# Kernel optimization log

Measured on AMD Instinct MI355X. Metric: run time of the kernel, lower is better.

## Reference

```python
import jax, jax.numpy as jnp
import numpy as np

N = 50000       # nodes
E = 800000      # edges (avg degree 16)
IN_DIM = 64
H = 64          # hidden_dim
OUT_DIM = 64
R = 8           # n_relations
L = 3           # n_layers
LN_EPS = 1e-5
NEG_SLOPE = 0.2


def _layer_norm(x, g, b):
    mu = jnp.mean(x, axis=-1, keepdims=True)
    var = jnp.mean((x - mu) ** 2, axis=-1, keepdims=True)
    return (x - mu) * jax.lax.rsqrt(var + LN_EPS) * g + b


def setup_inputs() -> dict:
    key = jax.random.key(0)
    ks = jax.random.split(key, 10)
    s = 0.05
    return {
        "x": jax.random.normal(ks[0], (N, IN_DIM), jnp.float32),
        "edge_index": jax.random.randint(ks[1], (2, E), 0, N),
        "edge_type": jax.random.randint(ks[2], (E,), 0, R),
        "W_in": jax.random.normal(ks[3], (H, IN_DIM), jnp.float32) * s,
        "b_in": jnp.zeros((H,), jnp.float32),
        "W_rel": jax.random.normal(ks[4], (R, H, H), jnp.float32) * s,   # no bias
        "W_gate": jax.random.normal(ks[5], (R, H, H), jnp.float32) * s,
        "b_gate": jnp.zeros((R, H), jnp.float32),
        "W_att": jax.random.normal(ks[6], (R, 2 * H), jnp.float32) * s,  # Linear(2H,1) per relation
        "b_att": jnp.zeros((R,), jnp.float32),
        "ln_gamma": jnp.ones((L, H), jnp.float32),
        "ln_beta": jnp.zeros((L, H), jnp.float32),
        "W_out": jax.random.normal(ks[7], (OUT_DIM, H), jnp.float32) * s,
        "b_out": jnp.zeros((OUT_DIM,), jnp.float32),
    }


def reference(x, edge_index, edge_type, W_in, b_in, W_rel, W_gate, b_gate,
              W_att, b_att, ln_gamma, ln_beta, W_out, b_out):
    src, dst = edge_index[0], edge_index[1]
    Wa_src, Wa_dst = W_att[:, :H], W_att[:, H:]      # [R,H] each
    seg = dst * R + edge_type                        # combined (node, relation) scatter key
    eidx = jnp.arange(E)

    h = jax.nn.relu(x @ W_in.T + b_in)               # [N,H]

    for layer in range(L):
        h_src = h[src]                               # [E,H] gather
        h_dst = h[dst]                               # [E,H] gather
        # attention score of each edge under its own relation's Linear(2H,1)
        scores_all = h_src @ Wa_src.T + h_dst @ Wa_dst.T + b_att   # [E,R]
        scores = scores_all[eidx, edge_type]                        # [E]
        scores = jax.nn.leaky_relu(scores, NEG_SLOPE)
        # softmax over dim=0 within each relation's edge set (as in the torch code)
        m = jax.ops.segment_max(scores, edge_type, num_segments=R)
        ex = jnp.exp(scores - m[edge_type])
        denom = jax.ops.segment_sum(ex, edge_type, num_segments=R)
        att = ex / denom[edge_type]                                 # [E]
        # relation-specific linear of source features (linear commutes with gather)
        hWr = jnp.einsum('nh,rkh->nrk', h, W_rel)                   # [N,R,H]
        msg = hWr[src, edge_type] * att[:, None]                    # [E,H]
        # per-relation scatter-add into destinations
        agg = jax.ops.segment_sum(msg, seg, num_segments=N * R)     # [N*R,H]
        agg = agg.reshape(N, R, H)
        gate = jax.nn.sigmoid(jnp.einsum('nh,rkh->nrk', h, W_gate) + b_gate)  # [N,R,H]
        h_new = jnp.mean(gate * agg, axis=1)         # sum(messages)/n_relations
        h = jax.nn.relu(_layer_norm(h + h_new, ln_gamma[layer], ln_beta[layer]))

    return h @ W_out.T + b_out
```

## Files before the change

kernel.cpp:

```cpp
#include <hip/hip_runtime.h>
#include <math.h>

#define NN 50000
#define EE 800000
#define HH 64
#define RR 8
#define LL 3
#define NR (NN * RR)
#define NB ((NR + 255) / 256)
#define LN_EPS 1e-5f
#define NEG_SLOPE 0.2f
#define LDH 68
#define PNB 584
#define OTB (16 * LDH)
#define DSPREAD 64

typedef __attribute__((ext_vector_type(8))) short bf8;
typedef __attribute__((ext_vector_type(4))) float f4;
typedef __attribute__((ext_vector_type(8))) unsigned short us8;
typedef __attribute__((ext_vector_type(2))) unsigned int u2;

__device__ __forceinline__ unsigned short bf16r(float f) {
    unsigned u = __float_as_uint(f);
    unsigned r = u + 0x7fffu + ((u >> 16) & 1u);
    return (unsigned short)(r >> 16);
}
__device__ __forceinline__ float bf2f(unsigned short u) {
    return __uint_as_float(((unsigned)u) << 16);
}

__global__ __launch_bounds__(256) void proj_in(
    const float* __restrict__ x, const float* __restrict__ W,
    const float* __restrict__ bias, const unsigned short* __restrict__ WaB,
    float* __restrict__ h, unsigned short* __restrict__ hbf,
    float* __restrict__ s_src, float* __restrict__ s_dst) {
    __shared__ float WT[64 * LDH];
    __shared__ float xs[16 * LDH];
    __shared__ float hs[16 * LDH];
    int tid = threadIdx.x;
    int n0 = blockIdx.x * 16;
    #pragma unroll
    for (int s = 0; s < 16; ++s) {
        int idx = tid + 256 * s;
        int k = idx >> 6, i = idx & 63;
        WT[i * LDH + k] = W[idx];
    }
    int row = tid >> 4, cg = tid & 15;
    {
        f4 v = ((const f4*)x)[(size_t)(n0 + row) * 16 + cg];
        *(f4*)&xs[row * LDH + cg * 4] = v;
    }
    __syncthreads();
    f4 acc;
    {
        f4 b = *(const f4*)(bias + cg * 4);
        acc = b;
        #pragma unroll
        for (int i = 0; i < 64; ++i) {
            float xv = xs[row * LDH + i];
            f4 wt = *(const f4*)&WT[i * LDH + cg * 4];
            acc[0] += xv * wt[0];
            acc[1] += xv * wt[1];
            acc[2] += xv * wt[2];
            acc[3] += xv * wt[3];
        }
        #pragma unroll
        for (int j = 0; j < 4; ++j) acc[j] = fmaxf(acc[j], 0.f);
        int n = n0 + row;
        *(f4*)(h + (size_t)n * 64 + cg * 4) = acc;
        u2 u;
        u[0] = (unsigned)bf16r(acc[0]) | ((unsigned)bf16r(acc[1]) << 16);
        u[1] = (unsigned)bf16r(acc[2]) | ((unsigned)bf16r(acc[3]) << 16);
        *(u2*)(hbf + (size_t)n * 64 + cg * 4) = u;
        *(f4*)&hs[row * LDH + cg * 4] = acc;
    }
    __syncthreads();
    if (tid < 64) {
        int lane = tid;
        int quad = lane >> 4, lr = lane & 15;
        f4 sc = (f4){0.f, 0.f, 0.f, 0.f};
        #pragma unroll
        for (int kb = 0; kb < 2; ++kb) {
            const float* p = &hs[lr * LDH + kb * 32 + quad * 8];
            bf8 a;
            #pragma unroll
            for (int j = 0; j < 8; ++j) a[j] = (short)bf16r(p[j]);
            const bf8* bw = (const bf8*)(WaB + lr * 64 + kb * 32 + quad * 8);
            sc = __builtin_amdgcn_mfma_f32_16x16x32_bf16(a, *bw, sc, 0, 0, 0);
        }
        #pragma unroll
        for (int j = 0; j < 4; ++j) {
            int n = n0 + quad * 4 + j;
            if (lr < 8) s_src[n * 8 + lr] = sc[j];
            else        s_dst[n * 8 + (lr - 8)] = sc[j];
        }
    }
}

__global__ void edge_count(const int* __restrict__ ei, const int* __restrict__ et,
                           int* __restrict__ counts, int* __restrict__ rank) {
    int e = blockIdx.x * 256 + threadIdx.x;
    int d = ei[EE + e], t = et[e];
    rank[e] = atomicAdd(&counts[d * 8 + t], 1);
}

__global__ void scan1(const int* __restrict__ counts, int* __restrict__ offs,
                      int* __restrict__ bsum) {
    __shared__ int s[256];
    int tid = threadIdx.x;
    int i = blockIdx.x * 256 + tid;
    int v = (i < NR) ? counts[i] : 0;
    s[tid] = v; __syncthreads();
    for (int d = 1; d < 256; d <<= 1) {
        int x = (tid >= d) ? s[tid - d] : 0;
        __syncthreads();
        s[tid] += x;
        __syncthreads();
    }
    if (i < NR) offs[i] = s[tid] - v;
    if (tid == 255) bsum[blockIdx.x] = s[255];
}

__global__ void scan2(int* __restrict__ bsum) {
    __shared__ int s[1024];
    int tid = threadIdx.x;
    int carry = 0;
    for (int c0 = 0; c0 < NB; c0 += 1024) {
        int i = c0 + tid;
        int v = (i < NB) ? bsum[i] : 0;
        s[tid] = v; __syncthreads();
        for (int d = 1; d < 1024; d <<= 1) {
            int x = (tid >= d) ? s[tid - d] : 0;
            __syncthreads();
            s[tid] += x;
            __syncthreads();
        }
        if (i < NB) bsum[i] = carry + s[tid] - v;
        int tot = s[1023];
        __syncthreads();
        carry += tot;
    }
}

__global__ void edge_fill(const int* __restrict__ ei, const int* __restrict__ et,
                          const int* __restrict__ rank, const int* __restrict__ offs,
                          const int* __restrict__ bsum, u2* __restrict__ spack) {
    int e = blockIdx.x * 256 + threadIdx.x;
    int s = ei[e], d = ei[EE + e], t = et[e];
    int seg = d * 8 + t;
    int slot = offs[seg] + bsum[seg >> 8] + rank[e];
    spack[slot] = (u2){(unsigned)s, (unsigned)seg};
}

__global__ void cvt_w(const float* __restrict__ Wr, const float* __restrict__ Wg,
                      const float* __restrict__ Wa, const float* __restrict__ Wo,
                      unsigned short* __restrict__ WrB, unsigned short* __restrict__ WgB,
                      unsigned short* __restrict__ WaB, unsigned short* __restrict__ WoB) {
    int i = blockIdx.x * 256 + threadIdx.x;
    WrB[i] = bf16r(Wr[i]);
    WgB[i] = bf16r(Wg[i]);
    if (i < 1024) {
        int row = i >> 6, k = i & 63;
        float v = (row < 8) ? Wa[row * 128 + k] : Wa[(row - 8) * 128 + 64 + k];
        WaB[i] = bf16r(v);
    }
    if (i < 4096) WoB[i] = bf16r(Wo[i]);
}

__global__ void edge_softmax2(const u2* __restrict__ spack,
                              const float* __restrict__ s_src, const float* __restrict__ s_dst,
                              const float* __restrict__ b_att,
                              u2* __restrict__ epack, float* __restrict__ dpart) {
    __shared__ float lsum[4][8];
    int tid = threadIdx.x;
    if (tid < 32) lsum[tid >> 3][tid & 7] = 0.f;
    __syncthreads();
    int slot = blockIdx.x * 256 + tid;
    u2 sp = spack[slot];
    int src = (int)sp[0];
    int seg = (int)sp[1];
    int t = seg & 7;
    float sc = s_src[src * 8 + t] + s_dst[seg] + b_att[t];
    sc = (sc >= 0.f) ? sc : NEG_SLOPE * sc;
    float ex = __expf(sc);
    epack[slot] = (u2){(unsigned)src, __float_as_uint(ex)};
    atomicAdd(&lsum[tid >> 6][t], ex);
    __syncthreads();
    if (tid < 8) {
        float v = lsum[0][tid] + lsum[1][tid] + lsum[2][tid] + lsum[3][tid];
        atomicAdd(&dpart[(blockIdx.x & (DSPREAD - 1)) * 16 + tid], v);
    }
}

template<bool EMIT, bool OUT>
__global__ __launch_bounds__(256, 6) void combine_fused(
    const float* __restrict__ hbuf, const unsigned short* __restrict__ hbf_in,
    const int* __restrict__ offs, const int* __restrict__ bsum,
    const u2* __restrict__ epack, const float* __restrict__ dpartL,
    const unsigned short* __restrict__ WrB, const unsigned short* __restrict__ WgB,
    const unsigned short* __restrict__ WaB, const unsigned short* __restrict__ WoB,
    const float* __restrict__ b_gate, const float* __restrict__ gamma,
    const float* __restrict__ beta, float* __restrict__ hout,
    unsigned short* __restrict__ hbf_out, float* __restrict__ ssrc_out,
    float* __restrict__ sdst_out, float* __restrict__ outp,
    const float* __restrict__ b_out) {
    __shared__ float hs[16 * LDH];
    __shared__ alignas(16) unsigned short ps[16 * PNB];
    __shared__ float idn8[8];
    __shared__ int offsL[129];
    float* ps_f = (float*)ps;
    int tid = threadIdx.x;
    int n0 = blockIdx.x * 16;

    {
        int row = tid >> 4, c4 = tid & 15;
        f4 v = ((const f4*)hbuf)[(size_t)(n0 + row) * 16 + c4];
        *(f4*)&hs[row * LDH + c4 * 4] = v;
    }
    if (tid < 129) {
        int sidx = n0 * 8 + tid;
        offsL[tid] = (sidx < NR) ? (offs[sidx] + bsum[sidx >> 8]) : EE;
    }
    if (tid >= 192) {
        int t = tid & 7, g = (tid - 192) >> 3;
        float sm = 0.f;
        #pragma unroll
        for (int j = 0; j < 8; ++j) sm += dpartL[(g * 8 + j) * 16 + t];
        sm += __shfl_xor(sm, 8, 64);
        sm += __shfl_xor(sm, 16, 64);
        sm += __shfl_xor(sm, 32, 64);
        if ((tid & 63) < 8) idn8[t] = 1.f / sm;
    }
    __syncthreads();

    {
        int segl = tid >> 1;
        int half = tid & 1;
        int lo = offsL[segl], hi = offsL[segl + 1];
        int r = segl & 7;
        int gn = segl >> 3;
        float fa[32];
        #pragma unroll
        for (int j = 0; j < 32; ++j) fa[j] = 0.f;
        for (int s = lo; s < hi; s += 2) {
            u2 pk0 = epack[s];
            int s1 = (s + 1 < hi) ? (s + 1) : s;
            u2 pk1 = epack[s1];
            float a0 = __uint_as_float(pk0[1]);
            float a1 = (s + 1 < hi) ? __uint_as_float(pk1[1]) : 0.f;
            const us8* hp0 = (const us8*)(hbf_in + ((size_t)(int)pk0[0] << 6) + half * 32);
            const us8* hp1 = (const us8*)(hbf_in + ((size_t)(int)pk1[0] << 6) + half * 32);
            #pragma unroll
            for (int q = 0; q < 4; ++q) {
                us8 v0 = hp0[q];
                us8 v1 = hp1[q];
                #pragma unroll
                for (int j = 0; j < 8; ++j) {
                    fa[q * 8 + j] += a0 * bf2f(v0[j]);
                    fa[q * 8 + j] += a1 * bf2f(v1[j]);
                }
            }
        }
        float sA = idn8[r];
        unsigned short* pp = &ps[gn * PNB + r * 72 + half * 32];
        #pragma unroll
        for (int q = 0; q < 4; ++q) {
            us8 o;
            #pragma unroll
            for (int j = 0; j < 8; ++j) o[j] = bf16r(fa[q * 8 + j] * sA);
            *(us8*)(pp + q * 8) = o;
        }
    }
    __syncthreads();

    int w = tid >> 6, lane = tid & 63;
    int quad = lane >> 4, lr = lane & 15;
    int tn = w;

    bf8 a_h[2];
    #pragma unroll
    for (int kb = 0; kb < 2; ++kb) {
        const float* p = &hs[lr * LDH + kb * 32 + quad * 8];
        bf8 a;
        #pragma unroll
        for (int j = 0; j < 8; ++j) a[j] = (short)bf16r(p[j]);
        a_h[kb] = a;
    }

    f4 acc = (f4){0.f, 0.f, 0.f, 0.f};
    for (int r = 0; r < 8; ++r) {
        bf8 a_p[2];
        #pragma unroll
        for (int kb = 0; kb < 2; ++kb)
            a_p[kb] = *(const bf8*)&ps[lr * PNB + r * 72 + kb * 32 + quad * 8];
        f4 aggc = (f4){0.f, 0.f, 0.f, 0.f};
        f4 gacc = (f4){0.f, 0.f, 0.f, 0.f};
        #pragma unroll
        for (int kb = 0; kb < 2; ++kb) {
            const bf8* br = (const bf8*)(WrB + ((r * 64 + tn * 16 + lr) * 64 + kb * 32 + quad * 8));
            const bf8* bg = (const bf8*)(WgB + ((r * 64 + tn * 16 + lr) * 64 + kb * 32 + quad * 8));
            aggc = __builtin_amdgcn_mfma_f32_16x16x32_bf16(a_p[kb], *br, aggc, 0, 0, 0);
            gacc = __builtin_amdgcn_mfma_f32_16x16x32_bf16(a_h[kb], *bg, gacc, 0, 0, 0);
        }
        float bg = b_gate[r * 64 + tn * 16 + lr];
        #pragma unroll
        for (int j = 0; j < 4; ++j) {
            float g = 1.f / (1.f + __expf(-(gacc[j] + bg)));
            acc[j] += g * aggc[j];
        }
    }
    __syncthreads();

    #pragma unroll
    for (int j = 0; j < 4; ++j) {
        int row = quad * 4 + j;
        int col = tn * 16 + lr;
        ps_f[row * LDH + col] = hs[row * LDH + col] + acc[j] * 0.125f;
    }
    __syncthreads();

    {
        int row = tid >> 4, c = tid & 15;
        int n = n0 + row;
        f4 tv = *(const f4*)&ps_f[row * LDH + c * 4];
        float s1 = tv[0] + tv[1] + tv[2] + tv[3];
        float s2 = tv[0]*tv[0] + tv[1]*tv[1] + tv[2]*tv[2] + tv[3]*tv[3];
        #pragma unroll
        for (int off = 1; off <= 8; off <<= 1) {
            s1 += __shfl_xor(s1, off, 64);
            s2 += __shfl_xor(s2, off, 64);
        }
        float mu = s1 * (1.f / 64.f);
        float var = s2 * (1.f / 64.f) - mu * mu;
        float rs = rsqrtf(var + LN_EPS);
        f4 g = *(const f4*)(gamma + c * 4);
        f4 b = *(const f4*)(beta + c * 4);
        f4 ov;
        #pragma unroll
        for (int j = 0; j < 4; ++j)
            ov[j] = fmaxf((tv[j] - mu) * rs * g[j] + b[j], 0.f);
        if (!OUT)
            *(f4*)(hout + (size_t)n * 64 + c * 4) = ov;
        *(f4*)&ps_f[OTB + row * LDH + c * 4] = ov;
        if (EMIT) {
            u2 u;
            u[0] = (unsigned)bf16r(ov[0]) | ((unsigned)bf16r(ov[1]) << 16);
            u[1] = (unsigned)bf16r(ov[2]) | ((unsigned)bf16r(ov[3]) << 16);
            *(u2*)(hbf_out + (size_t)n * 64 + c * 4) = u;
        }
    }

    if (EMIT) {
        __syncthreads();
        if (w == 0) {
            f4 sc = (f4){0.f, 0.f, 0.f, 0.f};
            #pragma unroll
            for (int kb = 0; kb < 2; ++kb) {
                const float* p = &ps_f[OTB + lr * LDH + kb * 32 + quad * 8];
                bf8 a;
                #pragma unroll
                for (int j = 0; j < 8; ++j) a[j] = (short)bf16r(p[j]);
                const bf8* bw = (const bf8*)(WaB + lr * 64 + kb * 32 + quad * 8);
                sc = __builtin_amdgcn_mfma_f32_16x16x32_bf16(a, *bw, sc, 0, 0, 0);
            }
            #pragma unroll
            for (int j = 0; j < 4; ++j) {
                int n = n0 + quad * 4 + j;
                if (lr < 8) ssrc_out[n * 8 + lr] = sc[j];
                else        sdst_out[n * 8 + (lr - 8)] = sc[j];
            }
        }
    }

    if (OUT) {
        __syncthreads();
        f4 oc = (f4){0.f, 0.f, 0.f, 0.f};
        #pragma unroll
        for (int kb = 0; kb < 2; ++kb) {
            const float* p = &ps_f[OTB + lr * LDH + kb * 32 + quad * 8];
            bf8 a;
            #pragma unroll
            for (int j = 0; j < 8; ++j) a[j] = (short)bf16r(p[j]);
            const bf8* bw = (const bf8*)(WoB + ((tn * 16 + lr) * 64 + kb * 32 + quad * 8));
            oc = __builtin_amdgcn_mfma_f32_16x16x32_bf16(a, *bw, oc, 0, 0, 0);
        }
        float bo = b_out[tn * 16 + lr];
        #pragma unroll
        for (int j = 0; j < 4; ++j)
            outp[(size_t)(n0 + quad * 4 + j) * 64 + tn * 16 + lr] = oc[j] + bo;
    }
}

extern "C" void kernel_launch(void* const* d_in, const int* in_sizes, int n_in,
                              void* d_out, int out_size, void* d_ws, size_t ws_size,
                              hipStream_t stream) {
    const float* x      = (const float*)d_in[0];
    const int*   ei     = (const int*)d_in[1];
    const int*   et     = (const int*)d_in[2];
    const float* W_in   = (const float*)d_in[3];
    const float* b_in   = (const float*)d_in[4];
    const float* W_rel  = (const float*)d_in[5];
    const float* W_gate = (const float*)d_in[6];
    const float* b_gate = (const float*)d_in[7];
    const float* W_att  = (const float*)d_in[8];
    const float* b_att  = (const float*)d_in[9];
    const float* ln_g   = (const float*)d_in[10];
    const float* ln_b   = (const float*)d_in[11];
    const float* W_out  = (const float*)d_in[12];
    const float* b_out  = (const float*)d_in[13];
    float* out = (float*)d_out;

    float* h0 = (float*)d_out;

    char* ws = (char*)d_ws;
    float* h1 = (float*)ws;                     ws += (size_t)NN * 64 * 4;
    unsigned short* hbfA = (unsigned short*)ws; ws += (size_t)NN * 64 * 2;
    unsigned short* hbfB = (unsigned short*)ws; ws += (size_t)NN * 64 * 2;
    float* s_src = (float*)ws;                  ws += (size_t)NN * 8 * 4;
    float* s_dst = (float*)ws;                  ws += (size_t)NN * 8 * 4;
    unsigned short* WrB = (unsigned short*)ws;  ws += (size_t)RR * 64 * 64 * 2;
    unsigned short* WgB = (unsigned short*)ws;  ws += (size_t)RR * 64 * 64 * 2;
    unsigned short* WaB = (unsigned short*)ws;  ws += 2048;
    unsigned short* WoB = (unsigned short*)ws;  ws += 8192;
    int* counts = (int*)ws;                     ws += (size_t)NR * 4;
    float* dpart = (float*)ws;                  ws += 3 * DSPREAD * 16 * 4;
    int* offs = (int*)ws;                       ws += (size_t)NR * 4;
    int* bsum = (int*)ws;                       ws += 6400;
    int* rank = (int*)ws;                       ws += (size_t)EE * 4;
    u2* spack = (u2*)ws;                        ws += (size_t)EE * 8;
    u2* epack = (u2*)ws;                        ws += (size_t)EE * 8;

    hipMemsetAsync(counts, 0, (size_t)NR * 4 + 3 * DSPREAD * 16 * 4, stream);
    cvt_w<<<128, 256, 0, stream>>>(W_rel, W_gate, W_att, W_out, WrB, WgB, WaB, WoB);
    edge_count<<<EE / 256, 256, 0, stream>>>(ei, et, counts, rank);
    scan1<<<NB, 256, 0, stream>>>(counts, offs, bsum);
    scan2<<<1, 1024, 0, stream>>>(bsum);
    edge_fill<<<EE / 256, 256, 0, stream>>>(ei, et, rank, offs, bsum, spack);
    proj_in<<<NN / 16, 256, 0, stream>>>(x, W_in, b_in, WaB, h0, hbfA, s_src, s_dst);

    const int tiles16 = NN / 16;
    float* hA = h0;  float* hB = h1;
    unsigned short* bfA = hbfA;  unsigned short* bfB = hbfB;
    for (int layer = 0; layer < LL; ++layer) {
        float* dpl = dpart + (size_t)layer * DSPREAD * 16;
        edge_softmax2<<<EE / 256, 256, 0, stream>>>(spack, s_src, s_dst, b_att,
                                                    epack, dpl);
        if (layer < LL - 1) {
            combine_fused<true, false><<<tiles16, 256, 0, stream>>>(
                hA, bfA, offs, bsum, epack, dpl, WrB, WgB, WaB, WoB, b_gate,
                ln_g + layer * 64, ln_b + layer * 64,
                hB, bfB, s_src, s_dst, out, b_out);
        } else {
            combine_fused<false, true><<<tiles16, 256, 0, stream>>>(
                hA, bfA, offs, bsum, epack, dpl, WrB, WgB, WaB, WoB, b_gate,
                ln_g + layer * 64, ln_b + layer * 64,
                hB, bfB, s_src, s_dst, out, b_out);
        }
        float* tf = hA; hA = hB; hB = tf;
        unsigned short* tb = bfA; bfA = bfB; bfB = tb;
    }
}
```

Baseline: 420.2 us.

## Aggregate edge messages per block with shared-memory atomics instead of per-segment threads

The combine kernel now assigns one thread per edge across the block's whole edge range and accumulates weighted source features into a shared fp32 tile [128 segments x 66] with LDS atomics. This replaces the old scheme where each pair of threads walked one (node, relation) segment serially. The goal is to fix load imbalance from uneven segment lengths. The softmax kernel now writes only the exp values, and the source index is read from the existing spack. In exchange there are 64 LDS atomic adds per edge, a larger shared buffer, and occupancy is lowered to 4 waves via launch bounds.

```diff
diff --git a/kernel.cpp b/kernel.cpp
--- a/kernel.cpp
+++ b/kernel.cpp
@@ -14,9 +14,11 @@
 #define PNB 584
 #define OTB (16 * LDH)
 #define DSPREAD 64
+#define SAG 66
 
 typedef __attribute__((ext_vector_type(8))) short bf8;
 typedef __attribute__((ext_vector_type(4))) float f4;
+typedef __attribute__((ext_vector_type(2))) float f2;
 typedef __attribute__((ext_vector_type(8))) unsigned short us8;
 typedef __attribute__((ext_vector_type(2))) unsigned int u2;
 
@@ -170,7 +172,7 @@
 __global__ void edge_softmax2(const u2* __restrict__ spack,
                               const float* __restrict__ s_src, const float* __restrict__ s_dst,
                               const float* __restrict__ b_att,
-                              u2* __restrict__ epack, float* __restrict__ dpart) {
+                              float* __restrict__ exw, float* __restrict__ dpart) {
     __shared__ float lsum[4][8];
     int tid = threadIdx.x;
     if (tid < 32) lsum[tid >> 3][tid & 7] = 0.f;
@@ -183,7 +185,7 @@
     float sc = s_src[src * 8 + t] + s_dst[seg] + b_att[t];
     sc = (sc >= 0.f) ? sc : NEG_SLOPE * sc;
     float ex = __expf(sc);
-    epack[slot] = (u2){(unsigned)src, __float_as_uint(ex)};
+    exw[slot] = ex;
     atomicAdd(&lsum[tid >> 6][t], ex);
     __syncthreads();
     if (tid < 8) {
@@ -193,10 +195,11 @@
 }
 
 template<bool EMIT, bool OUT>
-__global__ __launch_bounds__(256, 6) void combine_fused(
+__global__ __launch_bounds__(256, 4) void combine_fused(
     const float* __restrict__ hbuf, const unsigned short* __restrict__ hbf_in,
     const int* __restrict__ offs, const int* __restrict__ bsum,
-    const u2* __restrict__ epack, const float* __restrict__ dpartL,
+    const u2* __restrict__ spack, const float* __restrict__ exw,
+    const float* __restrict__ dpartL,
     const unsigned short* __restrict__ WrB, const unsigned short* __restrict__ WgB,
     const unsigned short* __restrict__ WaB, const unsigned short* __restrict__ WoB,
     const float* __restrict__ b_gate, const float* __restrict__ gamma,
@@ -205,10 +208,11 @@
     float* __restrict__ sdst_out, float* __restrict__ outp,
     const float* __restrict__ b_out) {
     __shared__ float hs[16 * LDH];
-    __shared__ alignas(16) unsigned short ps[16 * PNB];
+    __shared__ alignas(16) float agg[128 * SAG];
     __shared__ float idn8[8];
-    __shared__ int offsL[129];
-    float* ps_f = (float*)ps;
+    __shared__ int rng[2];
+    unsigned short* ps = (unsigned short*)agg;
+    float* ps_f = agg;
     int tid = threadIdx.x;
     int n0 = blockIdx.x * 16;
 
@@ -217,9 +221,9 @@
         f4 v = ((const f4*)hbuf)[(size_t)(n0 + row) * 16 + c4];
         *(f4*)&hs[row * LDH + c4 * 4] = v;
     }
-    if (tid < 129) {
-        int sidx = n0 * 8 + tid;
-        offsL[tid] = (sidx < NR) ? (offs[sidx] + bsum[sidx >> 8]) : EE;
+    if (tid < 2) {
+        int sidx = n0 * 8 + tid * 128;
+        rng[tid] = (sidx < NR) ? (offs[sidx] + bsum[sidx >> 8]) : EE;
     }
     if (tid >= 192) {
         int t = tid & 7, g = (tid - 192) >> 3;
@@ -231,43 +235,53 @@
         sm += __shfl_xor(sm, 32, 64);
         if ((tid & 63) < 8) idn8[t] = 1.f / sm;
     }
-    __syncthreads();
-
-    {
-        int segl = tid >> 1;
-        int half = tid & 1;
-        int lo = offsL[segl], hi = offsL[segl + 1];
-        int r = segl & 7;
-        int gn = segl >> 3;
-        float fa[32];
-        #pragma unroll
-        for (int j = 0; j < 32; ++j) fa[j] = 0.f;
-        for (int s = lo; s < hi; s += 2) {
-            u2 pk0 = epack[s];
-            int s1 = (s + 1 < hi) ? (s + 1) : s;
-            u2 pk1 = epack[s1];
-            float a0 = __uint_as_float(pk0[1]);
-            float a1 = (s + 1 < hi) ? __uint_as_float(pk1[1]) : 0.f;
-            const us8* hp0 = (const us8*)(hbf_in + ((size_t)(int)pk0[0] << 6) + half * 32);
-            const us8* hp1 = (const us8*)(hbf_in + ((size_t)(int)pk1[0] << 6) + half * 32);
-            #pragma unroll
-            for (int q = 0; q < 4; ++q) {
-                us8 v0 = hp0[q];
-                us8 v1 = hp1[q];
+    {
+        f4 z = (f4){0.f, 0.f, 0.f, 0.f};
+        for (int i = tid; i < (128 * SAG) / 4; i += 256) ((f4*)agg)[i] = z;
+    }
+    __syncthreads();
+
+    {
+        int lo0 = rng[0], hi0 = rng[1];
+        for (int s = lo0 + tid; s < hi0; s += 256) {
+            u2 sp = spack[s];
+            int src = (int)sp[0];
+            int abase = ((int)sp[1] - n0 * 8) * SAG;
+            float ex = exw[s];
+            const us8* hp = (const us8*)(hbf_in + ((size_t)src << 6));
+            #pragma unroll
+            for (int q = 0; q < 8; ++q) {
+                us8 v = hp[q];
                 #pragma unroll
-                for (int j = 0; j < 8; ++j) {
-                    fa[q * 8 + j] += a0 * bf2f(v0[j]);
-                    fa[q * 8 + j] += a1 * bf2f(v1[j]);
-                }
+                for (int j = 0; j < 8; ++j)
+                    atomicAdd(&agg[abase + q * 8 + j], ex * bf2f(v[j]));
             }
         }
+    }
+    __syncthreads();
+
+    float fr[32];
+    {
+        int segl = tid >> 1, half = tid & 1;
+        const float* ar = &agg[segl * SAG + half * 32];
+        #pragma unroll
+        for (int j = 0; j < 16; ++j) {
+            f2 v = *(const f2*)(ar + 2 * j);
+            fr[2 * j]     = v[0];
+            fr[2 * j + 1] = v[1];
+        }
+    }
+    __syncthreads();
+    {
+        int segl = tid >> 1, half = tid & 1;
+        int r = segl & 7, gn = segl >> 3;
         float sA = idn8[r];
         unsigned short* pp = &ps[gn * PNB + r * 72 + half * 32];
         #pragma unroll
         for (int q = 0; q < 4; ++q) {
             us8 o;
             #pragma unroll
-            for (int j = 0; j < 8; ++j) o[j] = bf16r(fa[q * 8 + j] * sA);
+            for (int j = 0; j < 8; ++j) o[j] = bf16r(fr[q * 8 + j] * sA);
             *(us8*)(pp + q * 8) = o;
         }
     }
@@ -428,7 +442,7 @@
     int* bsum = (int*)ws;                       ws += 6400;
     int* rank = (int*)ws;                       ws += (size_t)EE * 4;
     u2* spack = (u2*)ws;                        ws += (size_t)EE * 8;
-    u2* epack = (u2*)ws;                        ws += (size_t)EE * 8;
+    float* exw = (float*)ws;                    ws += (size_t)EE * 4;
 
     hipMemsetAsync(counts, 0, (size_t)NR * 4 + 3 * DSPREAD * 16 * 4, stream);
     cvt_w<<<128, 256, 0, stream>>>(W_rel, W_gate, W_att, W_out, WrB, WgB, WaB, WoB);
@@ -444,15 +458,15 @@
     for (int layer = 0; layer < LL; ++layer) {
         float* dpl = dpart + (size_t)layer * DSPREAD * 16;
         edge_softmax2<<<EE / 256, 256, 0, stream>>>(spack, s_src, s_dst, b_att,
-                                                    epack, dpl);
+                                                    exw, dpl);
         if (layer < LL - 1) {
             combine_fused<true, false><<<tiles16, 256, 0, stream>>>(
-                hA, bfA, offs, bsum, epack, dpl, WrB, WgB, WaB, WoB, b_gate,
+                hA, bfA, offs, bsum, spack, exw, dpl, WrB, WgB, WaB, WoB, b_gate,
                 ln_g + layer * 64, ln_b + layer * 64,
                 hB, bfB, s_src, s_dst, out, b_out);
         } else {
             combine_fused<false, true><<<tiles16, 256, 0, stream>>>(
-                hA, bfA, offs, bsum, epack, dpl, WrB, WgB, WaB, WoB, b_gate,
+                hA, bfA, offs, bsum, spack, exw, dpl, WrB, WgB, WaB, WoB, b_gate,
                 ln_g + layer * 64, ln_b + layer * 64,
                 hB, bfB, s_src, s_dst, out, b_out);
         }
```

Result: slower. 1.228 ms (+192.2%).

## Split fused combine into separate gather kernel and dense MFMA combine kernel

Applied to the files above, without the earlier changes.

The edge gather/aggregation phase moves out of the fused combine kernel into a new gather_seg kernel. It writes per-(node,relation) aggregated bf16 rows to a global buffer, which combine_dense then reads directly as MFMA operands. The gather also unpacks bf16 pairs with bit masks into float2 FMAs. The split frees LDS and registers in each kernel, which may raise occupancy and separate irregular memory traffic from dense compute. In exchange it adds a global round trip of N*R*64 bf16 values and an extra launch per layer.

```diff
diff --git a/kernel.cpp b/kernel.cpp
--- a/kernel.cpp
+++ b/kernel.cpp
@@ -11,14 +11,15 @@
 #define LN_EPS 1e-5f
 #define NEG_SLOPE 0.2f
 #define LDH 68
-#define PNB 584
 #define OTB (16 * LDH)
 #define DSPREAD 64
 
 typedef __attribute__((ext_vector_type(8))) short bf8;
 typedef __attribute__((ext_vector_type(4))) float f4;
+typedef __attribute__((ext_vector_type(2))) float f2;
 typedef __attribute__((ext_vector_type(8))) unsigned short us8;
 typedef __attribute__((ext_vector_type(2))) unsigned int u2;
+typedef __attribute__((ext_vector_type(4))) unsigned int u4;
 
 __device__ __forceinline__ unsigned short bf16r(float f) {
     unsigned u = __float_as_uint(f);
@@ -192,11 +193,77 @@
     }
 }
 
-template<bool EMIT, bool OUT>
-__global__ __launch_bounds__(256, 6) void combine_fused(
-    const float* __restrict__ hbuf, const unsigned short* __restrict__ hbf_in,
+__global__ __launch_bounds__(256, 6) void gather_seg(
     const int* __restrict__ offs, const int* __restrict__ bsum,
     const u2* __restrict__ epack, const float* __restrict__ dpartL,
+    const unsigned short* __restrict__ hbf_in,
+    unsigned short* __restrict__ psG) {
+    int tid = threadIdx.x;
+    int segl = tid >> 1, half = tid & 1;
+    int sidx = blockIdx.x * 128 + segl;
+    int lo = offs[sidx] + bsum[sidx >> 8];
+    int nxt = sidx + 1;
+    int hi = (nxt < NR) ? (offs[nxt] + bsum[nxt >> 8]) : EE;
+
+    int lane = tid & 63;
+    float sm = 0.f;
+    #pragma unroll
+    for (int k = 0; k < 8; ++k)
+        sm += dpartL[(((lane >> 3) + 8 * k) * 16) + (lane & 7)];
+    sm += __shfl_xor(sm, 8, 64);
+    sm += __shfl_xor(sm, 16, 64);
+    sm += __shfl_xor(sm, 32, 64);
+    float rc = 1.f / sm;
+    float idn = __shfl(rc, segl & 7, 64);
+
+    f2 acc[16];
+    #pragma unroll
+    for (int i = 0; i < 16; ++i) acc[i] = (f2){0.f, 0.f};
+
+    for (int s = lo; s < hi; s += 2) {
+        u2 pk0 = epack[s];
+        int s1 = (s + 1 < hi) ? (s + 1) : s;
+        u2 pk1 = epack[s1];
+        float a0 = __uint_as_float(pk0[1]);
+        float a1 = (s + 1 < hi) ? __uint_as_float(pk1[1]) : 0.f;
+        const u4* hp0 = (const u4*)(hbf_in + ((size_t)(int)pk0[0] << 6) + half * 32);
+        const u4* hp1 = (const u4*)(hbf_in + ((size_t)(int)pk1[0] << 6) + half * 32);
+        f2 va0 = (f2){a0, a0};
+        f2 va1 = (f2){a1, a1};
+        #pragma unroll
+        for (int q = 0; q < 4; ++q) {
+            u4 d0 = hp0[q];
+            u4 d1 = hp1[q];
+            #pragma unroll
+            for (int k = 0; k < 4; ++k) {
+                f2 w0, w1;
+                w0[0] = __uint_as_float(d0[k] << 16);
+                w0[1] = __uint_as_float(d0[k] & 0xffff0000u);
+                w1[0] = __uint_as_float(d1[k] << 16);
+                w1[1] = __uint_as_float(d1[k] & 0xffff0000u);
+                acc[q * 4 + k] += va0 * w0;
+                acc[q * 4 + k] += va1 * w1;
+            }
+        }
+    }
+
+    int gn = segl >> 3, r = segl & 7;
+    unsigned short* pp = psG + ((((size_t)blockIdx.x * 16 + gn) * 8 + r) << 6) + half * 32;
+    #pragma unroll
+    for (int q = 0; q < 4; ++q) {
+        us8 o;
+        #pragma unroll
+        for (int k = 0; k < 4; ++k) {
+            o[2 * k]     = bf16r(acc[q * 4 + k][0] * idn);
+            o[2 * k + 1] = bf16r(acc[q * 4 + k][1] * idn);
+        }
+        *(us8*)(pp + q * 8) = o;
+    }
+}
+
+template<bool EMIT, bool OUT>
+__global__ __launch_bounds__(256, 6) void combine_dense(
+    const float* __restrict__ hbuf, const unsigned short* __restrict__ psG,
     const unsigned short* __restrict__ WrB, const unsigned short* __restrict__ WgB,
     const unsigned short* __restrict__ WaB, const unsigned short* __restrict__ WoB,
     const float* __restrict__ b_gate, const float* __restrict__ gamma,
@@ -205,10 +272,7 @@
     float* __restrict__ sdst_out, float* __restrict__ outp,
     const float* __restrict__ b_out) {
     __shared__ float hs[16 * LDH];
-    __shared__ alignas(16) unsigned short ps[16 * PNB];
-    __shared__ float idn8[8];
-    __shared__ int offsL[129];
-    float* ps_f = (float*)ps;
+    __shared__ float tf[32 * LDH];
     int tid = threadIdx.x;
     int n0 = blockIdx.x * 16;
 
@@ -217,60 +281,6 @@
         f4 v = ((const f4*)hbuf)[(size_t)(n0 + row) * 16 + c4];
         *(f4*)&hs[row * LDH + c4 * 4] = v;
     }
-    if (tid < 129) {
-        int sidx = n0 * 8 + tid;
-        offsL[tid] = (sidx < NR) ? (offs[sidx] + bsum[sidx >> 8]) : EE;
-    }
-    if (tid >= 192) {
-        int t = tid & 7, g = (tid - 192) >> 3;
-        float sm = 0.f;
-        #pragma unroll
-        for (int j = 0; j < 8; ++j) sm += dpartL[(g * 8 + j) * 16 + t];
-        sm += __shfl_xor(sm, 8, 64);
-        sm += __shfl_xor(sm, 16, 64);
-        sm += __shfl_xor(sm, 32, 64);
-        if ((tid & 63) < 8) idn8[t] = 1.f / sm;
-    }
-    __syncthreads();
-
-    {
-        int segl = tid >> 1;
-        int half = tid & 1;
-        int lo = offsL[segl], hi = offsL[segl + 1];
-        int r = segl & 7;
-        int gn = segl >> 3;
-        float fa[32];
-        #pragma unroll
-        for (int j = 0; j < 32; ++j) fa[j] = 0.f;
-        for (int s = lo; s < hi; s += 2) {
-            u2 pk0 = epack[s];
-            int s1 = (s + 1 < hi) ? (s + 1) : s;
-            u2 pk1 = epack[s1];
-            float a0 = __uint_as_float(pk0[1]);
-            float a1 = (s + 1 < hi) ? __uint_as_float(pk1[1]) : 0.f;
-            const us8* hp0 = (const us8*)(hbf_in + ((size_t)(int)pk0[0] << 6) + half * 32);
-            const us8* hp1 = (const us8*)(hbf_in + ((size_t)(int)pk1[0] << 6) + half * 32);
-            #pragma unroll
-            for (int q = 0; q < 4; ++q) {
-                us8 v0 = hp0[q];
-                us8 v1 = hp1[q];
-                #pragma unroll
-                for (int j = 0; j < 8; ++j) {
-                    fa[q * 8 + j] += a0 * bf2f(v0[j]);
-                    fa[q * 8 + j] += a1 * bf2f(v1[j]);
-                }
-            }
-        }
-        float sA = idn8[r];
-        unsigned short* pp = &ps[gn * PNB + r * 72 + half * 32];
-        #pragma unroll
-        for (int q = 0; q < 4; ++q) {
-            us8 o;
-            #pragma unroll
-            for (int j = 0; j < 8; ++j) o[j] = bf16r(fa[q * 8 + j] * sA);
-            *(us8*)(pp + q * 8) = o;
-        }
-    }
     __syncthreads();
 
     int w = tid >> 6, lane = tid & 63;
@@ -287,12 +297,14 @@
         a_h[kb] = a;
     }
 
+    const unsigned short* pbase =
+        psG + (((size_t)blockIdx.x * 16 + lr) << 9);
     f4 acc = (f4){0.f, 0.f, 0.f, 0.f};
     for (int r = 0; r < 8; ++r) {
         bf8 a_p[2];
         #pragma unroll
         for (int kb = 0; kb < 2; ++kb)
-            a_p[kb] = *(const bf8*)&ps[lr * PNB + r * 72 + kb * 32 + quad * 8];
+            a_p[kb] = *(const bf8*)(pbase + r * 64 + kb * 32 + quad * 8);
         f4 aggc = (f4){0.f, 0.f, 0.f, 0.f};
         f4 gacc = (f4){0.f, 0.f, 0.f, 0.f};
         #pragma unroll
@@ -309,20 +321,19 @@
             acc[j] += g * aggc[j];
         }
     }
-    __syncthreads();
 
     #pragma unroll
     for (int j = 0; j < 4; ++j) {
         int row = quad * 4 + j;
         int col = tn * 16 + lr;
-        ps_f[row * LDH + col] = hs[row * LDH + col] + acc[j] * 0.125f;
+        tf[row * LDH + col] = hs[row * LDH + col] + acc[j] * 0.125f;
     }
     __syncthreads();
 
     {
         int row = tid >> 4, c = tid & 15;
         int n = n0 + row;
-        f4 tv = *(const f4*)&ps_f[row * LDH + c * 4];
+        f4 tv = *(const f4*)&tf[row * LDH + c * 4];
         float s1 = tv[0] + tv[1] + tv[2] + tv[3];
         float s2 = tv[0]*tv[0] + tv[1]*tv[1] + tv[2]*tv[2] + tv[3]*tv[3];
         #pragma unroll
@@ -341,7 +352,7 @@
             ov[j] = fmaxf((tv[j] - mu) * rs * g[j] + b[j], 0.f);
         if (!OUT)
             *(f4*)(hout + (size_t)n * 64 + c * 4) = ov;
-        *(f4*)&ps_f[OTB + row * LDH + c * 4] = ov;
+        *(f4*)&tf[OTB + row * LDH + c * 4] = ov;
         if (EMIT) {
             u2 u;
             u[0] = (unsigned)bf16r(ov[0]) | ((unsigned)bf16r(ov[1]) << 16);
@@ -356,7 +367,7 @@
             f4 sc = (f4){0.f, 0.f, 0.f, 0.f};
             #pragma unroll
             for (int kb = 0; kb < 2; ++kb) {
-                const float* p = &ps_f[OTB + lr * LDH + kb * 32 + quad * 8];
+                const float* p = &tf[OTB + lr * LDH + kb * 32 + quad * 8];
                 bf8 a;
                 #pragma unroll
                 for (int j = 0; j < 8; ++j) a[j] = (short)bf16r(p[j]);
@@ -377,7 +388,7 @@
         f4 oc = (f4){0.f, 0.f, 0.f, 0.f};
         #pragma unroll
         for (int kb = 0; kb < 2; ++kb) {
-            const float* p = &ps_f[OTB + lr * LDH + kb * 32 + quad * 8];
+            const float* p = &tf[OTB + lr * LDH + kb * 32 + quad * 8];
             bf8 a;
             #pragma unroll
             for (int j = 0; j < 8; ++j) a[j] = (short)bf16r(p[j]);
@@ -429,6 +440,7 @@
     int* rank = (int*)ws;                       ws += (size_t)EE * 4;
     u2* spack = (u2*)ws;                        ws += (size_t)EE * 8;
     u2* epack = (u2*)ws;                        ws += (size_t)EE * 8;
+    unsigned short* psG = (unsigned short*)ws;  ws += (size_t)NR * 64 * 2;
 
     hipMemsetAsync(counts, 0, (size_t)NR * 4 + 3 * DSPREAD * 16 * 4, stream);
     cvt_w<<<128, 256, 0, stream>>>(W_rel, W_gate, W_att, W_out, WrB, WgB, WaB, WoB);
@@ -445,14 +457,15 @@
         float* dpl = dpart + (size_t)layer * DSPREAD * 16;
         edge_softmax2<<<EE / 256, 256, 0, stream>>>(spack, s_src, s_dst, b_att,
                                                     epack, dpl);
+        gather_seg<<<tiles16, 256, 0, stream>>>(offs, bsum, epack, dpl, bfA, psG);
         if (layer < LL - 1) {
-            combine_fused<true, false><<<tiles16, 256, 0, stream>>>(
-                hA, bfA, offs, bsum, epack, dpl, WrB, WgB, WaB, WoB, b_gate,
+            combine_dense<true, false><<<tiles16, 256, 0, stream>>>(
+                hA, psG, WrB, WgB, WaB, WoB, b_gate,
                 ln_g + layer * 64, ln_b + layer * 64,
                 hB, bfB, s_src, s_dst, out, b_out);
         } else {
-            combine_fused<false, true><<<tiles16, 256, 0, stream>>>(
-                hA, bfA, offs, bsum, epack, dpl, WrB, WgB, WaB, WoB, b_gate,
+            combine_dense<false, true><<<tiles16, 256, 0, stream>>>(
+                hA, psG, WrB, WgB, WaB, WoB, b_gate,
                 ln_g + layer * 64, ln_b + layer * 64,
                 hB, bfB, s_src, s_dst, out, b_out);
         }
```

Measured after the change: 541.9 us. +29.0%, slower.
